# Kernel tuning notes

Hardware: AMD Instinct MI355X
Metric: run time of the kernel (lower is better)

## Reference

```python
import jax, jax.numpy as jnp
import numpy as np

EPS = 1e-12
H = 256
W = 256
RANK = 4
CTX = 1024
BATCH = 32
FF = (H + W) * RANK * 4  # 8192
STD = 0.001


def _norm(x, axis):
    # torch: (x - mean) / sqrt(var(unbiased) + eps)
    m = jnp.mean(x, axis=axis, keepdims=True)
    v = jnp.var(x, axis=axis, keepdims=True, ddof=1)
    return (x - m) / jnp.sqrt(v + EPS)


def _norm_polar(x):
    # x: [B, N, 2]; magnitude-normalize relative to per-batch max magnitude
    x_abs = jnp.sqrt(x[..., 0] ** 2 + x[..., 1] ** 2 + EPS)          # [B, N]
    h = x_abs / (jnp.max(x_abs, axis=-1, keepdims=True) + EPS)       # [B, N]
    xn = x / (x_abs[..., None] + EPS)                                # [B, N, 2]
    return jnp.stack([h * xn[..., 0], h * xn[..., 1]], axis=-1)


def setup_inputs() -> dict:
    key = jax.random.key(0)
    ks = jax.random.split(key, 12)

    def lin(k, fan_in, shape):
        b = 1.0 / np.sqrt(fan_in)
        return jax.random.uniform(k, shape, jnp.float32, -b, b)

    weights_static = jnp.concatenate([
        jax.random.normal(ks[9], (1, H, W, 2), jnp.float32) * STD,
        jax.random.normal(ks[10], (1, H, W, 2), jnp.float32) * STD
        + jnp.array([1.0, 0.0], jnp.float32),
    ], axis=0)  # [2, H, W, 2]

    return {
        "x": jax.random.normal(ks[0], (BATCH, CTX), jnp.float32),
        "W_in": lin(ks[1], CTX, (FF, CTX)),
        "b_in": lin(ks[2], CTX, (FF,)),
        "W_gate": lin(ks[3], CTX, (FF, CTX)),
        "b_gate": lin(ks[4], CTX, (FF,)),
        "W_t": lin(ks[5], FF, (FF, FF)),
        "b_t": lin(ks[6], FF, (FF,)),
        "conv_w": lin(ks[7], RANK, (RANK, RANK)),  # 1x1 conv kernel [out, in]
        "conv_b": lin(ks[8], RANK, (RANK,)),
        "weights_static": weights_static,
        "weights_mod": jax.random.normal(ks[11], (4, H, W), jnp.float32) * STD,
    }


def reference(x, W_in, b_in, W_gate, b_gate, W_t, b_t, conv_w, conv_b,
              weights_static, weights_mod):
    b = x.shape[0]
    # dual linear projections (dropout p=0 -> identity)
    xt = x @ W_in.T + b_in            # [B, FF]
    xg = x @ W_gate.T + b_gate        # [B, FF]
    stack = jnp.stack([xt, xg], axis=0).reshape(2, b, 4, -1)
    stack = _norm(stack, -1)
    ctx = (stack[0] * jnp.tanh(stack[1])).reshape(b, -1)   # gated, [B, FF]
    ctx = ctx @ W_t.T + b_t                                 # [B, FF]
    ctx = ctx.reshape(b, 4, RANK, H + W)
    modc = _norm(ctx, -1)
    # outer product -> [B, 4, RANK, H, W]
    mod = jnp.tanh(jnp.einsum('bkri,bkrj->bkrij', modc[..., :H], modc[..., H:]))
    # channel 0: 1x1 conv over rank channels, then sum channels (keepdim)
    mod_real = jnp.einsum('oi,bihw->bohw', conv_w, mod[:, 0]) + conv_b[None, :, None, None]
    mod_real = jnp.sum(mod_real, axis=1, keepdims=True)     # [B, 1, H, W]
    mod_other = jnp.sum(mod[:, 1:], axis=2)                 # [B, 3, H, W]
    mod = jnp.concatenate([mod_real, mod_other], axis=1)    # [B, 4, H, W]
    mod = weights_mod[None] * mod

    A0 = weights_static[0]            # [H, W, 2]
    A1 = weights_static[1]            # [H, W, 2]
    Bm = jnp.moveaxis(mod[:, 0:2], 1, -1)                   # [B, H, W, 2]
    ms_r = A1[..., 0] * Bm[..., 0] - A1[..., 1] * Bm[..., 1]
    ms_i = A1[..., 0] * Bm[..., 1] - A1[..., 1] * Bm[..., 0]
    mod_scaled = jnp.stack([ms_r, ms_i], axis=-1)           # [B, H, W, 2]
    mod_scaled = _norm_polar(mod_scaled.reshape(b, H * W, 2)).reshape(b, H, W, 2)

    mag = jnp.sqrt(mod_scaled[..., 0] ** 2 + mod_scaled[..., 1] ** 2 + EPS)
    mag = jnp.sqrt(jnp.mean(mag, axis=(-1, -2)) + EPS)      # [B]
    mod_scaled = mod_scaled / mag[:, None, None, None]

    mod_weights = A0[None] + mod_scaled                     # [B, H, W, 2]

    mod_proj = jnp.moveaxis(mod[:, 2:], 1, -1)              # [B, H, W, 2]
    mod_proj = _norm_polar(mod_proj.reshape(b, H * W, 2)).reshape(b, H, W, 2)
    den = jnp.sqrt(mod_proj[..., 0] ** 2 + mod_proj[..., 1] ** 2 + EPS)
    theta_cos = mod_proj[..., 0] / den
    theta_sin = mod_proj[..., 1] / den
    weights = mod_weights[..., 0] * theta_cos + mod_weights[..., 1] * theta_sin
    return weights  # [B, H, W]
```

## Files before the change

kernel.cpp:

```cpp
#include <hip/hip_runtime.h>
#include <cstddef>

#define NB   32
#define CTXD 1024
#define FFD  8192
#define HD   256
#define WD   256
#define NPIX 65536
#define EPSF 1e-12f

typedef __attribute__((ext_vector_type(8))) short bf16x8;
typedef __attribute__((ext_vector_type(4))) float f32x4;


__device__ __forceinline__ float ftanh(float x){
  float ax = fabsf(x);
  float e  = __expf(2.0f*ax);
  float r  = 1.0f - 2.0f*__builtin_amdgcn_rcpf(e + 1.0f);
  return copysignf(r, x);
}

__device__ __forceinline__ unsigned short f2bf(float f){
  unsigned u = __float_as_uint(f);
  unsigned r = (u + 0x7FFFu + ((u >> 16) & 1u)) >> 16;
  return (unsigned short)r;
}
__device__ __forceinline__ float bf2f(unsigned short s){
  return __uint_as_float((unsigned)s << 16);
}

__device__ __forceinline__ void split3(float f, unsigned short& s0,
                                       unsigned short& s1, unsigned short& s2){
  s0 = f2bf(f);
  float r1 = f - bf2f(s0);
  s1 = f2bf(r1);
  float r2 = r1 - bf2f(s1);
  s2 = f2bf(r2);
}

__device__ __forceinline__ void block_reduce4(float& a, float& b, float& c, float& d){
  for (int off = 32; off > 0; off >>= 1){
    a += __shfl_down(a, off); b += __shfl_down(b, off);
    c += __shfl_down(c, off); d += __shfl_down(d, off);
  }
  __shared__ float lds[16];
  int wid = threadIdx.x >> 6, lane = threadIdx.x & 63;
  if (lane == 0){ lds[wid*4+0]=a; lds[wid*4+1]=b; lds[wid*4+2]=c; lds[wid*4+3]=d; }
  __syncthreads();
  a = (lds[0]+lds[4])+(lds[8]+lds[12]);
  b = (lds[1]+lds[5])+(lds[9]+lds[13]);
  c = (lds[2]+lds[6])+(lds[10]+lds[14]);
  d = (lds[3]+lds[7])+(lds[11]+lds[15]);
}


__global__ __launch_bounds__(256) void k_prep(
    const float* __restrict__ x, unsigned short* __restrict__ P,
    float* __restrict__ red){
  int g = blockIdx.x*256 + threadIdx.x;
  if (g < 64) red[g] = 0.0f;
  int b = g >> 7, grp = g & 127;
  int koff = grp*8;
  int c = grp >> 2, kg = grp & 3;
  const float* src = x + (size_t)b*CTXD + koff;
  float4 v0 = *(const float4*)(src), v1 = *(const float4*)(src+4);
  float vv[8] = {v0.x,v0.y,v0.z,v0.w,v1.x,v1.y,v1.z,v1.w};
  bf16x8 a0, a1, a2;
  #pragma unroll
  for (int e = 0; e < 8; ++e){
    unsigned short s0,s1,s2; split3(vv[e],s0,s1,s2);
    a0[e]=(short)s0; a1[e]=(short)s1; a2[e]=(short)s2;
  }
  size_t base = (size_t)c*3072 + (b>>4)*512 + kg*128 + (b&15)*8;
  *(bf16x8*)(P + base)        = a0;
  *(bf16x8*)(P + base + 1024) = a1;
  *(bf16x8*)(P + base + 2048) = a2;
}

template<int KC>
__global__ __launch_bounds__(256) void k_gemm_mfma(
    const float* __restrict__ W0, const float* __restrict__ W1,
    const unsigned short* __restrict__ BP,
    float* __restrict__ Cp, int K, size_t zstride){
  const float* __restrict__ W = blockIdx.z ? W1 : W0;
  int wave = threadIdx.x >> 6;
  int lane = threadIdx.x & 63;
  int f0   = blockIdx.x*64 + wave*16;
  int kc   = blockIdx.y;
  int row  = lane & 15;
  int kg   = lane >> 4;
  int rot  = blockIdx.x & (KC-1);
  const float* Wb = W + (size_t)(f0+row)*K + kc*KC*32 + kg*8;
  const unsigned short* Bb = BP + (size_t)kc*KC*3072 + kg*128 + row*8;
  f32x4 acc0={0.f,0.f,0.f,0.f}, acc1={0.f,0.f,0.f,0.f};
  const float* wp = Wb + rot*32;
  float4 w0 = *(const float4*)(wp), w1 = *(const float4*)(wp+4);
  for (int c = 0; c < KC; ++c){
    int rc = (c + rot) & (KC-1);
    const unsigned short* bp = Bb + (size_t)rc*3072;
    bf16x8 b0h0 = *(const bf16x8*)(bp);
    bf16x8 b0h1 = *(const bf16x8*)(bp +  512);
    bf16x8 b1h0 = *(const bf16x8*)(bp + 1024);
    bf16x8 b1h1 = *(const bf16x8*)(bp + 1536);
    bf16x8 b2h0 = *(const bf16x8*)(bp + 2048);
    bf16x8 b2h1 = *(const bf16x8*)(bp + 2560);
    float4 cw0 = w0, cw1 = w1;
    if (c + 1 < KC){
      int rn = (c + 1 + rot) & (KC-1);
      wp = Wb + rn*32;
      w0 = *(const float4*)(wp); w1 = *(const float4*)(wp+4);
    }
    bf16x8 a0, a1, a2;
    float wv[8] = {cw0.x,cw0.y,cw0.z,cw0.w,cw1.x,cw1.y,cw1.z,cw1.w};
    #pragma unroll
    for (int e = 0; e < 8; ++e){
      unsigned short s0,s1,s2; split3(wv[e],s0,s1,s2);
      a0[e]=(short)s0; a1[e]=(short)s1; a2[e]=(short)s2;
    }
    acc0 = __builtin_amdgcn_mfma_f32_16x16x32_bf16(a0, b0h0, acc0, 0,0,0);
    acc1 = __builtin_amdgcn_mfma_f32_16x16x32_bf16(a0, b0h1, acc1, 0,0,0);
    acc0 = __builtin_amdgcn_mfma_f32_16x16x32_bf16(a0, b1h0, acc0, 0,0,0);
    acc1 = __builtin_amdgcn_mfma_f32_16x16x32_bf16(a0, b1h1, acc1, 0,0,0);
    acc0 = __builtin_amdgcn_mfma_f32_16x16x32_bf16(a1, b0h0, acc0, 0,0,0);
    acc1 = __builtin_amdgcn_mfma_f32_16x16x32_bf16(a1, b0h1, acc1, 0,0,0);
    acc0 = __builtin_amdgcn_mfma_f32_16x16x32_bf16(a0, b2h0, acc0, 0,0,0);
    acc1 = __builtin_amdgcn_mfma_f32_16x16x32_bf16(a0, b2h1, acc1, 0,0,0);
    acc0 = __builtin_amdgcn_mfma_f32_16x16x32_bf16(a1, b1h0, acc0, 0,0,0);
    acc1 = __builtin_amdgcn_mfma_f32_16x16x32_bf16(a1, b1h1, acc1, 0,0,0);
    acc0 = __builtin_amdgcn_mfma_f32_16x16x32_bf16(a2, b0h0, acc0, 0,0,0);
    acc1 = __builtin_amdgcn_mfma_f32_16x16x32_bf16(a2, b0h1, acc1, 0,0,0);
  }
  float* __restrict__ C = Cp + (size_t)blockIdx.z*zstride + (size_t)kc*(FFD*32);
  #pragma unroll
  for (int r = 0; r < 4; ++r){
    int f = f0 + kg*4 + r;
    C[(size_t)f*32 + row]      = acc0[r];
    C[(size_t)f*32 + 16 + row] = acc1[r];
  }
}

__global__ __launch_bounds__(256) void k_reduce1(
    const float* __restrict__ Cp, const float* __restrict__ bin,
    const float* __restrict__ bg, float* __restrict__ xtT,
    float* __restrict__ xgT){
  int g = blockIdx.x*256 + threadIdx.x;
  int m = g >> 18, idx = g & 262143;
  int f = idx >> 5;
  const float* __restrict__ cp = Cp + (size_t)m*(8ull*FFD*32);
  float s = (m ? bg : bin)[f];
  #pragma unroll
  for (int sI = 0; sI < 8; ++sI) s += cp[(size_t)sI*(FFD*32) + idx];
  (m ? xgT : xtT)[idx] = s;
}

__global__ __launch_bounds__(256) void k_reduce2(
    const float* __restrict__ Cp, const float* __restrict__ bias,
    float* __restrict__ outT){
  int g = blockIdx.x*256 + threadIdx.x;
  int f = g >> 5;
  float s = bias[f];
  #pragma unroll
  for (int sI = 0; sI < 16; ++sI) s += Cp[(size_t)sI*(FFD*32) + g];
  outT[g] = s;
}

__global__ __launch_bounds__(256) void k_normgate(
    const float* __restrict__ xtT, const float* __restrict__ xgT,
    unsigned short* __restrict__ P){
  int b = blockIdx.x >> 2, g4 = blockIdx.x & 3;
  int t = threadIdx.x;
  int f8 = g4*2048 + t*8;
  float vt[8], vg[8];
  float st=0.f, sst=0.f, sg=0.f, ssg=0.f;
  #pragma unroll
  for (int i = 0; i < 8; ++i){
    int f = f8 + i;
    float a = xtT[(size_t)f*NB + b];
    float c = xgT[(size_t)f*NB + b];
    vt[i]=a; vg[i]=c;
    st += a; sst += a*a; sg += c; ssg += c*c;
  }
  block_reduce4(st, sst, sg, ssg);
  float mt = st * (1.0f/2048.0f);
  float it = rsqrtf((sst - st*mt) * (1.0f/2047.0f) + EPSF);
  float mg = sg * (1.0f/2048.0f);
  float ig = rsqrtf((ssg - sg*mg) * (1.0f/2047.0f) + EPSF);
  bf16x8 a0, a1, a2;
  #pragma unroll
  for (int i = 0; i < 8; ++i){
    float nt = (vt[i]-mt)*it;
    float ng = (vg[i]-mg)*ig;
    float cv = nt * ftanh(ng);
    unsigned short s0,s1,s2; split3(cv,s0,s1,s2);
    a0[i]=(short)s0; a1[i]=(short)s1; a2[i]=(short)s2;
  }
  int c2 = f8 >> 5, kg = (f8 >> 3) & 3;
  size_t base = (size_t)c2*3072 + (b>>4)*512 + kg*128 + (b&15)*8;
  *(bf16x8*)(P + base)        = a0;
  *(bf16x8*)(P + base + 1024) = a1;
  *(bf16x8*)(P + base + 2048) = a2;
}

__global__ __launch_bounds__(256) void k_norm512(
    const float* __restrict__ ctx2T, float* __restrict__ modc){
  int b = blockIdx.x >> 4, kr = blockIdx.x & 15;
  int t = threadIdx.x;
  int base = kr*512;
  float v0 = ctx2T[(base + t      )*NB + b];
  float v1 = ctx2T[(base + 256 + t)*NB + b];
  float s = v0+v1, ss = v0*v0 + v1*v1, d0=0.f, d1=0.f;
  block_reduce4(s, ss, d0, d1);
  float m   = s * (1.0f/512.0f);
  float inv = rsqrtf((ss - s*m) * (1.0f/511.0f) + EPSF);
  modc[b*FFD + base + t      ] = (v0-m)*inv;
  modc[b*FFD + base + 256 + t] = (v1-m)*inv;
}

__global__ __launch_bounds__(256) void k_pixel1(
    const float* __restrict__ modc,
    const float* __restrict__ convw, const float* __restrict__ convb,
    const float* __restrict__ wmod, const float* __restrict__ wstat,
    float* __restrict__ msr, float* __restrict__ msi,
    float* __restrict__ ppr, float* __restrict__ ppi,
    float* __restrict__ red){
  int b = blockIdx.x >> 4, chunk = blockIdx.x & 15;
  int t = threadIdx.x;
  __shared__ float lds[16*512];
  #pragma unroll
  for (int i = 0; i < 8; ++i){
    float4 v = *(const float4*)(modc + (size_t)b*FFD + (i*256 + t)*4);
    *(float4*)(lds + (i*256 + t)*4) = v;
  }
  float cw0 = convw[0]+convw[4]+convw[8]+convw[12];
  float cw1 = convw[1]+convw[5]+convw[9]+convw[13];
  float cw2 = convw[2]+convw[6]+convw[10]+convw[14];
  float cw3 = convw[3]+convw[7]+convw[11]+convw[15];
  float cb  = convb[0]+convb[1]+convb[2]+convb[3];
  __syncthreads();
  int w = t;
  float mxs = 0.f, mxp = 0.f;
  for (int it = 0; it < 16; ++it){
    int h = chunk*16 + it;
    int pix = h*WD + w;
    float sk[4];
    #pragma unroll
    for (int k = 0; k < 4; ++k){
      float acc = 0.f;
      #pragma unroll
      for (int r = 0; r < 4; ++r){
        int kr = k*4 + r;
        float u  = lds[kr*512 + h];
        float vv = lds[kr*512 + 256 + w];
        float tt = ftanh(u*vv);
        float cwr = (r==0)?cw0:(r==1)?cw1:(r==2)?cw2:cw3;
        acc += (k==0) ? cwr*tt : tt;
      }
      sk[k] = acc;
    }
    sk[0] += cb;
    float m0 = sk[0]*wmod[0*NPIX+pix];
    float m1 = sk[1]*wmod[1*NPIX+pix];
    float m2 = sk[2]*wmod[2*NPIX+pix];
    float m3 = sk[3]*wmod[3*NPIX+pix];
    float2 A1 = *(const float2*)(wstat + (size_t)(NPIX + pix)*2);
    float r_ = A1.x*m0 - A1.y*m1;
    float i_ = A1.x*m1 - A1.y*m0;
    size_t o = (size_t)b*NPIX + pix;
    msr[o]=r_; msi[o]=i_; ppr[o]=m2; ppi[o]=m3;
    float as = sqrtf(r_*r_ + i_*i_ + EPSF);
    float ap = sqrtf(m2*m2 + m3*m3 + EPSF);
    mxs = fmaxf(mxs, as); mxp = fmaxf(mxp, ap);
  }
  for (int off = 32; off > 0; off >>= 1){
    mxs = fmaxf(mxs, __shfl_down(mxs, off));
    mxp = fmaxf(mxp, __shfl_down(mxp, off));
  }
  __shared__ float lred[8];
  int wid = t >> 6, lane = t & 63;
  if (lane == 0){ lred[wid] = mxs; lred[4+wid] = mxp; }
  __syncthreads();
  if (t == 0){
    float a = fmaxf(fmaxf(lred[0],lred[1]), fmaxf(lred[2],lred[3]));
    float p = fmaxf(fmaxf(lred[4],lred[5]), fmaxf(lred[6],lred[7]));
    atomicMax((int*)&red[b],    __float_as_int(a));
    atomicMax((int*)&red[32+b], __float_as_int(p));
  }
}

__global__ __launch_bounds__(256) void k_magsum(
    const float* __restrict__ msr, const float* __restrict__ msi,
    const float* __restrict__ red, float* __restrict__ magpart){
  int b = blockIdx.x >> 5, chunk = blockIdx.x & 31;
  int t = threadIdx.x;
  float maxs = red[b];
  float sum = 0.f;
  #pragma unroll
  for (int i = 0; i < 8; ++i){
    int pix = chunk*2048 + i*256 + t;
    size_t o = (size_t)b*NPIX + pix;
    float r_ = msr[o], i_ = msi[o];
    float sq = r_*r_ + i_*i_;
    float as = sqrtf(sq + EPSF);
    float hs = as/(maxs + EPSF);
    float tt = hs/(as + EPSF);
    sum += sqrtf(tt*tt*sq + EPSF);
  }
  for (int off = 32; off > 0; off >>= 1) sum += __shfl_down(sum, off);
  __shared__ float lr[4];
  int wid = t >> 6, lane = t & 63;
  if (lane == 0) lr[wid] = sum;
  __syncthreads();
  if (t == 0) magpart[b*32 + chunk] = (lr[0]+lr[1])+(lr[2]+lr[3]);
}

__global__ __launch_bounds__(256) void k_final(
    const float* __restrict__ msr, const float* __restrict__ msi,
    const float* __restrict__ ppr, const float* __restrict__ ppi,
    const float* __restrict__ wstat, const float* __restrict__ red,
    const float* __restrict__ magpart, float* __restrict__ out){
  int g = blockIdx.x*256 + threadIdx.x;
  int b = g >> 16, pix = g & (NPIX-1);
  __shared__ float s_im;
  if (threadIdx.x < 32){
    float v = magpart[b*32 + threadIdx.x];
    for (int off = 16; off > 0; off >>= 1) v += __shfl_down(v, off);
    if (threadIdx.x == 0) s_im = rsqrtf(v*(1.0f/65536.0f) + EPSF);
  }
  __syncthreads();
  float im = s_im;
  size_t o = (size_t)b*NPIX + pix;
  float maxs = red[b], maxp = red[32+b];
  float r_ = msr[o], i_ = msi[o], p_ = ppr[o], q_ = ppi[o];
  float as = sqrtf(r_*r_ + i_*i_ + EPSF);
  float fs = (as/(maxs+EPSF))/(as+EPSF)*im;
  float2 A0 = *(const float2*)(wstat + (size_t)pix*2);
  float mwr = A0.x + fs*r_;
  float mwi = A0.y + fs*i_;
  float ap = sqrtf(p_*p_ + q_*q_ + EPSF);
  float fp = (ap/(maxp+EPSF))/(ap+EPSF);
  float mpr = fp*p_, mpi = fp*q_;
  float den = sqrtf(mpr*mpr + mpi*mpi + EPSF);
  out[o] = (mwr*mpr + mwi*mpi)/den;
}


extern "C" void kernel_launch(void* const* d_in, const int* in_sizes, int n_in,
                              void* d_out, int out_size, void* d_ws, size_t ws_size,
                              hipStream_t stream){
  const float* x     = (const float*)d_in[0];
  const float* Win   = (const float*)d_in[1];
  const float* bin   = (const float*)d_in[2];
  const float* Wg    = (const float*)d_in[3];
  const float* bg    = (const float*)d_in[4];
  const float* Wt    = (const float*)d_in[5];
  const float* bt    = (const float*)d_in[6];
  const float* convw = (const float*)d_in[7];
  const float* convb = (const float*)d_in[8];
  const float* wstat = (const float*)d_in[9];
  const float* wmod  = (const float*)d_in[10];
  float* out = (float*)d_out;
  float* ws  = (float*)d_ws;

  float* xtT   = ws;
  float* xgT   = ws + 262144;
  unsigned short* P2 = (unsigned short*)(ws + 524288);
  unsigned short* P1 = (unsigned short*)(ws + 917504);
  float* ctx2T = ws;
  float* modc  = ws + 262144;
  float* msr   = ws + 966656;
  float* msi   = ws + 3063808;
  float* ppr   = ws + 5160960;
  float* ppi   = ws + 7258112;
  float* red     = ws + 9355264;
  float* magpart = ws + 9355328;

  float* Cp2 = msr;
  float* Cp1 = ppr;

  k_prep<<<16, 256, 0, stream>>>(x, P1, red);
  k_gemm_mfma<4><<<dim3(128,8,2), 256, 0, stream>>>(Win, Wg, P1,
                                                    Cp1, CTXD, 8ull*FFD*32);
  k_reduce1<<<2048, 256, 0, stream>>>(Cp1, bin, bg, xtT, xgT);
  k_normgate<<<128, 256, 0, stream>>>(xtT, xgT, P2);
  k_gemm_mfma<16><<<dim3(128,16,1), 256, 0, stream>>>(Wt, Wt, P2,
                                                      Cp2, FFD, 0);
  k_reduce2<<<1024, 256, 0, stream>>>(Cp2, bt, ctx2T);
  k_norm512<<<512, 256, 0, stream>>>(ctx2T, modc);
  k_pixel1<<<512, 256, 0, stream>>>(modc, convw, convb, wmod, wstat,
                                    msr, msi, ppr, ppi, red);
  k_magsum<<<1024, 256, 0, stream>>>(msr, msi, red, magpart);
  k_final<<<8192, 256, 0, stream>>>(msr, msi, ppr, ppi, wstat, red, magpart, out);
}
```

Measured before the change: 175.9 us.

## Recompute pixel modulation in scan and final passes instead of storing intermediates

Replaces the pixel pass that stored four full-resolution intermediate arrays with a scan kernel that only computes per-batch maxima and magnitude sums. The final kernel recomputes the per-pixel tanh/conv modulation from the cached LDS vectors. The magnitude mean is derived algebraically from the sum of raw magnitudes divided by the max, removing the separate magsum kernel. This trades large global memory writes and reads for doubled tanh arithmetic, and slightly changes the eps handling in the magnitude mean.

```diff
diff --git a/kernel.cpp b/kernel.cpp
--- a/kernel.cpp
+++ b/kernel.cpp
@@ -51,6 +51,37 @@
   b = (lds[1]+lds[5])+(lds[9]+lds[13]);
   c = (lds[2]+lds[6])+(lds[10]+lds[14]);
   d = (lds[3]+lds[7])+(lds[11]+lds[15]);
+}
+
+__device__ __forceinline__ void pixel_core(
+    const float* __restrict__ lds, int h, int w, int pix,
+    float cw0, float cw1, float cw2, float cw3, float cb,
+    const float* __restrict__ wmod, const float* __restrict__ wstat,
+    float& r_, float& i_, float& p_, float& q_){
+  float sk[4];
+  #pragma unroll
+  for (int k = 0; k < 4; ++k){
+    float acc = 0.f;
+    #pragma unroll
+    for (int r = 0; r < 4; ++r){
+      int kr = k*4 + r;
+      float u  = lds[kr*512 + h];
+      float vv = lds[kr*512 + 256 + w];
+      float tt = ftanh(u*vv);
+      float cwr = (r==0)?cw0:(r==1)?cw1:(r==2)?cw2:cw3;
+      acc += (k==0) ? cwr*tt : tt;
+    }
+    sk[k] = acc;
+  }
+  sk[0] += cb;
+  float m0 = sk[0]*wmod[0*NPIX+pix];
+  float m1 = sk[1]*wmod[1*NPIX+pix];
+  float m2 = sk[2]*wmod[2*NPIX+pix];
+  float m3 = sk[3]*wmod[3*NPIX+pix];
+  float2 A1 = *(const float2*)(wstat + (size_t)(NPIX + pix)*2);
+  r_ = A1.x*m0 - A1.y*m1;
+  i_ = A1.x*m1 - A1.y*m0;
+  p_ = m2; q_ = m3;
 }
 
 
@@ -216,13 +247,11 @@
   modc[b*FFD + base + 256 + t] = (v1-m)*inv;
 }
 
-__global__ __launch_bounds__(256) void k_pixel1(
+__global__ __launch_bounds__(256) void k_scan(
     const float* __restrict__ modc,
     const float* __restrict__ convw, const float* __restrict__ convb,
     const float* __restrict__ wmod, const float* __restrict__ wstat,
-    float* __restrict__ msr, float* __restrict__ msi,
-    float* __restrict__ ppr, float* __restrict__ ppi,
-    float* __restrict__ red){
+    float* __restrict__ red, float* __restrict__ magpart){
   int b = blockIdx.x >> 4, chunk = blockIdx.x & 15;
   int t = threadIdx.x;
   __shared__ float lds[16*512];
@@ -238,109 +267,86 @@
   float cb  = convb[0]+convb[1]+convb[2]+convb[3];
   __syncthreads();
   int w = t;
-  float mxs = 0.f, mxp = 0.f;
+  float mxs = 0.f, mxp = 0.f, sas = 0.f;
   for (int it = 0; it < 16; ++it){
     int h = chunk*16 + it;
     int pix = h*WD + w;
-    float sk[4];
-    #pragma unroll
-    for (int k = 0; k < 4; ++k){
-      float acc = 0.f;
-      #pragma unroll
-      for (int r = 0; r < 4; ++r){
-        int kr = k*4 + r;
-        float u  = lds[kr*512 + h];
-        float vv = lds[kr*512 + 256 + w];
-        float tt = ftanh(u*vv);
-        float cwr = (r==0)?cw0:(r==1)?cw1:(r==2)?cw2:cw3;
-        acc += (k==0) ? cwr*tt : tt;
-      }
-      sk[k] = acc;
-    }
-    sk[0] += cb;
-    float m0 = sk[0]*wmod[0*NPIX+pix];
-    float m1 = sk[1]*wmod[1*NPIX+pix];
-    float m2 = sk[2]*wmod[2*NPIX+pix];
-    float m3 = sk[3]*wmod[3*NPIX+pix];
-    float2 A1 = *(const float2*)(wstat + (size_t)(NPIX + pix)*2);
-    float r_ = A1.x*m0 - A1.y*m1;
-    float i_ = A1.x*m1 - A1.y*m0;
-    size_t o = (size_t)b*NPIX + pix;
-    msr[o]=r_; msi[o]=i_; ppr[o]=m2; ppi[o]=m3;
+    float r_, i_, p_, q_;
+    pixel_core(lds, h, w, pix, cw0, cw1, cw2, cw3, cb, wmod, wstat,
+               r_, i_, p_, q_);
     float as = sqrtf(r_*r_ + i_*i_ + EPSF);
-    float ap = sqrtf(m2*m2 + m3*m3 + EPSF);
+    float ap = sqrtf(p_*p_ + q_*q_ + EPSF);
     mxs = fmaxf(mxs, as); mxp = fmaxf(mxp, ap);
+    sas += as;
   }
   for (int off = 32; off > 0; off >>= 1){
     mxs = fmaxf(mxs, __shfl_down(mxs, off));
     mxp = fmaxf(mxp, __shfl_down(mxp, off));
-  }
-  __shared__ float lred[8];
+    sas += __shfl_down(sas, off);
+  }
+  __shared__ float lred[12];
   int wid = t >> 6, lane = t & 63;
-  if (lane == 0){ lred[wid] = mxs; lred[4+wid] = mxp; }
+  if (lane == 0){ lred[wid] = mxs; lred[4+wid] = mxp; lred[8+wid] = sas; }
   __syncthreads();
   if (t == 0){
     float a = fmaxf(fmaxf(lred[0],lred[1]), fmaxf(lred[2],lred[3]));
     float p = fmaxf(fmaxf(lred[4],lred[5]), fmaxf(lred[6],lred[7]));
+    float s = (lred[8]+lred[9])+(lred[10]+lred[11]);
     atomicMax((int*)&red[b],    __float_as_int(a));
     atomicMax((int*)&red[32+b], __float_as_int(p));
-  }
-}
-
-__global__ __launch_bounds__(256) void k_magsum(
-    const float* __restrict__ msr, const float* __restrict__ msi,
-    const float* __restrict__ red, float* __restrict__ magpart){
-  int b = blockIdx.x >> 5, chunk = blockIdx.x & 31;
+    magpart[b*16 + chunk] = s;
+  }
+}
+
+__global__ __launch_bounds__(256) void k_final(
+    const float* __restrict__ modc,
+    const float* __restrict__ convw, const float* __restrict__ convb,
+    const float* __restrict__ wmod, const float* __restrict__ wstat,
+    const float* __restrict__ red, const float* __restrict__ magpart,
+    float* __restrict__ out){
+  int b = blockIdx.x >> 4, chunk = blockIdx.x & 15;
   int t = threadIdx.x;
-  float maxs = red[b];
-  float sum = 0.f;
+  __shared__ float lds[16*512];
+  __shared__ float s_im;
+  if (t < 16){
+    float v = magpart[b*16 + t];
+    for (int off = 8; off > 0; off >>= 1) v += __shfl_down(v, off);
+    if (t == 0){
+      float maxs = red[b];
+      s_im = rsqrtf(v*(1.0f/65536.0f)/(maxs + EPSF) + EPSF);
+    }
+  }
   #pragma unroll
   for (int i = 0; i < 8; ++i){
-    int pix = chunk*2048 + i*256 + t;
-    size_t o = (size_t)b*NPIX + pix;
-    float r_ = msr[o], i_ = msi[o];
-    float sq = r_*r_ + i_*i_;
-    float as = sqrtf(sq + EPSF);
-    float hs = as/(maxs + EPSF);
-    float tt = hs/(as + EPSF);
-    sum += sqrtf(tt*tt*sq + EPSF);
-  }
-  for (int off = 32; off > 0; off >>= 1) sum += __shfl_down(sum, off);
-  __shared__ float lr[4];
-  int wid = t >> 6, lane = t & 63;
-  if (lane == 0) lr[wid] = sum;
-  __syncthreads();
-  if (t == 0) magpart[b*32 + chunk] = (lr[0]+lr[1])+(lr[2]+lr[3]);
-}
-
-__global__ __launch_bounds__(256) void k_final(
-    const float* __restrict__ msr, const float* __restrict__ msi,
-    const float* __restrict__ ppr, const float* __restrict__ ppi,
-    const float* __restrict__ wstat, const float* __restrict__ red,
-    const float* __restrict__ magpart, float* __restrict__ out){
-  int g = blockIdx.x*256 + threadIdx.x;
-  int b = g >> 16, pix = g & (NPIX-1);
-  __shared__ float s_im;
-  if (threadIdx.x < 32){
-    float v = magpart[b*32 + threadIdx.x];
-    for (int off = 16; off > 0; off >>= 1) v += __shfl_down(v, off);
-    if (threadIdx.x == 0) s_im = rsqrtf(v*(1.0f/65536.0f) + EPSF);
-  }
+    float4 v = *(const float4*)(modc + (size_t)b*FFD + (i*256 + t)*4);
+    *(float4*)(lds + (i*256 + t)*4) = v;
+  }
+  float cw0 = convw[0]+convw[4]+convw[8]+convw[12];
+  float cw1 = convw[1]+convw[5]+convw[9]+convw[13];
+  float cw2 = convw[2]+convw[6]+convw[10]+convw[14];
+  float cw3 = convw[3]+convw[7]+convw[11]+convw[15];
+  float cb  = convb[0]+convb[1]+convb[2]+convb[3];
   __syncthreads();
   float im = s_im;
-  size_t o = (size_t)b*NPIX + pix;
   float maxs = red[b], maxp = red[32+b];
-  float r_ = msr[o], i_ = msi[o], p_ = ppr[o], q_ = ppi[o];
-  float as = sqrtf(r_*r_ + i_*i_ + EPSF);
-  float fs = (as/(maxs+EPSF))/(as+EPSF)*im;
-  float2 A0 = *(const float2*)(wstat + (size_t)pix*2);
-  float mwr = A0.x + fs*r_;
-  float mwi = A0.y + fs*i_;
-  float ap = sqrtf(p_*p_ + q_*q_ + EPSF);
-  float fp = (ap/(maxp+EPSF))/(ap+EPSF);
-  float mpr = fp*p_, mpi = fp*q_;
-  float den = sqrtf(mpr*mpr + mpi*mpi + EPSF);
-  out[o] = (mwr*mpr + mwi*mpi)/den;
+  int w = t;
+  for (int it = 0; it < 16; ++it){
+    int h = chunk*16 + it;
+    int pix = h*WD + w;
+    float r_, i_, p_, q_;
+    pixel_core(lds, h, w, pix, cw0, cw1, cw2, cw3, cb, wmod, wstat,
+               r_, i_, p_, q_);
+    float as = sqrtf(r_*r_ + i_*i_ + EPSF);
+    float fs = (as/(maxs+EPSF))/(as+EPSF)*im;
+    float2 A0 = *(const float2*)(wstat + (size_t)pix*2);
+    float mwr = A0.x + fs*r_;
+    float mwi = A0.y + fs*i_;
+    float ap = sqrtf(p_*p_ + q_*q_ + EPSF);
+    float fp = (ap/(maxp+EPSF))/(ap+EPSF);
+    float mpr = fp*p_, mpi = fp*q_;
+    float den = sqrtf(mpr*mpr + mpi*mpi + EPSF);
+    out[(size_t)b*NPIX + pix] = (mwr*mpr + mwi*mpi)/den;
+  }
 }
 
 
@@ -363,31 +369,24 @@
 
   float* xtT   = ws;
   float* xgT   = ws + 262144;
+  float* ctx2T = ws;
+  float* modc  = ws + 262144;
   unsigned short* P2 = (unsigned short*)(ws + 524288);
   unsigned short* P1 = (unsigned short*)(ws + 917504);
-  float* ctx2T = ws;
-  float* modc  = ws + 262144;
-  float* msr   = ws + 966656;
-  float* msi   = ws + 3063808;
-  float* ppr   = ws + 5160960;
-  float* ppi   = ws + 7258112;
-  float* red     = ws + 9355264;
-  float* magpart = ws + 9355328;
-
-  float* Cp2 = msr;
-  float* Cp1 = ppr;
+  float* Cp    = ws + 966656;
+  float* red     = ws + 5160960;
+  float* magpart = ws + 5161024;
 
   k_prep<<<16, 256, 0, stream>>>(x, P1, red);
   k_gemm_mfma<4><<<dim3(128,8,2), 256, 0, stream>>>(Win, Wg, P1,
-                                                    Cp1, CTXD, 8ull*FFD*32);
-  k_reduce1<<<2048, 256, 0, stream>>>(Cp1, bin, bg, xtT, xgT);
+                                                    Cp, CTXD, 8ull*FFD*32);
+  k_reduce1<<<2048, 256, 0, stream>>>(Cp, bin, bg, xtT, xgT);
   k_normgate<<<128, 256, 0, stream>>>(xtT, xgT, P2);
   k_gemm_mfma<16><<<dim3(128,16,1), 256, 0, stream>>>(Wt, Wt, P2,
-                                                      Cp2, FFD, 0);
-  k_reduce2<<<1024, 256, 0, stream>>>(Cp2, bt, ctx2T);
+                                                      Cp, FFD, 0);
+  k_reduce2<<<1024, 256, 0, stream>>>(Cp, bt, ctx2T);
   k_norm512<<<512, 256, 0, stream>>>(ctx2T, modc);
-  k_pixel1<<<512, 256, 0, stream>>>(modc, convw, convb, wmod, wstat,
-                                    msr, msi, ppr, ppi, red);
-  k_magsum<<<1024, 256, 0, stream>>>(msr, msi, red, magpart);
-  k_final<<<8192, 256, 0, stream>>>(msr, msi, ppr, ppi, wstat, red, magpart, out);
-}
+  k_scan<<<512, 256, 0, stream>>>(modc, convw, convb, wmod, wstat, red, magpart);
+  k_final<<<512, 256, 0, stream>>>(modc, convw, convb, wmod, wstat, red,
+                                   magpart, out);
+}
```

Measured after the change: 174.0 us. Within noise of the previous version (-1.1%).
